# Performance work log

Hardware: AMD Instinct MI355X
Metric: run time of the kernel (lower is better)

## Reference

```python
import jax, jax.numpy as jnp
import numpy as np

DIM = 256

def setup_inputs() -> dict:
    key = jax.random.key(0)
    ks = jax.random.split(key, 7)
    B, S, D = 8, 4096, DIM
    scale = 1.0 / np.sqrt(D)
    x = jax.random.normal(ks[0], (B, S, D), dtype=jnp.float32)
    # torch Linear: y = x @ W.T + b, W is [out, in]
    Wq = jax.random.normal(ks[1], (D, D), dtype=jnp.float32) * scale
    Wk = jax.random.normal(ks[2], (D, D), dtype=jnp.float32) * scale
    Wv = jax.random.normal(ks[3], (D, D), dtype=jnp.float32) * scale
    bq = jax.random.normal(ks[4], (D,), dtype=jnp.float32) * 0.01
    bk = jax.random.normal(ks[5], (D,), dtype=jnp.float32) * 0.01
    bv = jax.random.normal(ks[6], (D,), dtype=jnp.float32) * 0.01
    return {"x": x, "Wq": Wq, "bq": bq, "Wk": Wk, "bk": bk, "Wv": Wv, "bv": bv}

def reference(x, Wq, bq, Wk, bk, Wv, bv):
    D = x.shape[-1]
    scale = D ** -0.5
    q = jnp.einsum('bsd,ed->bse', x, Wq) + bq  # [B,S,D]
    k = jnp.einsum('bsd,ed->bse', x, Wk) + bk
    v = jnp.einsum('bsd,ed->bse', x, Wv) + bv
    attn = jnp.einsum('bqd,bkd->bqk', q, k) * scale  # [B,S,S]
    attn = jax.nn.softmax(attn, axis=-1)
    return x + jnp.einsum('bqk,bkd->bqd', attn, v)
```

## Files before the change

kernel.cpp:

```cpp
#include <hip/hip_runtime.h>
#include <hip/hip_bf16.h>

typedef __attribute__((ext_vector_type(8))) short bf16x8;
typedef __attribute__((ext_vector_type(4))) short short4v;
typedef __attribute__((ext_vector_type(4))) float f32x4;
typedef __attribute__((ext_vector_type(16))) float f32x16;

#define MFMA16(a, b, c) __builtin_amdgcn_mfma_f32_16x16x32_bf16(a, b, c, 0, 0, 0)
#define MFMA32(a, b, c) __builtin_amdgcn_mfma_f32_32x32x16_bf16(a, b, c, 0, 0, 0)

__device__ __forceinline__ short f2bf(float f) {
    union { __hip_bfloat16 h; short s; } u;
    u.h = __float2bfloat16(f);
    return u.s;
}

__device__ __forceinline__ bf16x8 cvt8(const float* __restrict__ p) {
    f32x4 a = *reinterpret_cast<const f32x4*>(p);
    f32x4 b = *reinterpret_cast<const f32x4*>(p + 4);
    bf16x8 r;
    r[0] = f2bf(a[0]); r[1] = f2bf(a[1]); r[2] = f2bf(a[2]); r[3] = f2bf(a[3]);
    r[4] = f2bf(b[0]); r[5] = f2bf(b[1]); r[6] = f2bf(b[2]); r[7] = f2bf(b[3]);
    return r;
}

typedef __attribute__((address_space(1))) const unsigned int g_u32;
typedef __attribute__((address_space(3))) unsigned int l_u32;
__device__ __forceinline__ void gld16(const void* g, void* l) {
    __builtin_amdgcn_global_load_lds((g_u32*)(g), (l_u32*)(l), 16, 0, 0);
}

#define SBAR()    asm volatile("s_barrier" ::: "memory")
#define VMCNT(N)  asm volatile("s_waitcnt vmcnt(" #N ")" ::: "memory")

__global__ void wcvt_kernel(const float* __restrict__ Wq, const float* __restrict__ Wk,
                            const float* __restrict__ Wv, short* __restrict__ Wb)
{
    int t = blockIdx.x * 256 + threadIdx.x;
    int out_row = t & 255;
    int h  = (t >> 8) & 1;
    int kc = (t >> 9) & 15;
    int proj = t >> 13;
    const float* src = (proj == 0 ? Wq : (proj == 1 ? Wk : Wv))
                     + out_row * 256 + kc * 16 + h * 8;
    *reinterpret_cast<bf16x8*>(Wb + t * 8) = cvt8(src);
}

__global__ __launch_bounds__(256, 2) void qkv_kernel(
    const float* __restrict__ x, const short* __restrict__ Wb,
    const float* __restrict__ bq, const float* __restrict__ bk, const float* __restrict__ bv,
    short* __restrict__ qo, short* __restrict__ ko, short* __restrict__ vto)
{
    const int wave = threadIdx.x >> 6, lane = threadIdx.x & 63;
    const int l31 = lane & 31, h = lane >> 5;
    const int row0 = blockIdx.x * 128;
    const int wrow = row0 + wave * 32;

    bf16x8 af[16];
    const float* __restrict__ xr = x + (size_t)(wrow + l31) * 256 + h * 8;
#pragma unroll
    for (int kc = 0; kc < 16; ++kc) af[kc] = cvt8(xr + kc * 16);

    __shared__ short tile[128][264];

    for (int proj = 0; proj < 3; ++proj) {
        const short* __restrict__ W = Wb + proj * 65536;
        const float* __restrict__ bias = proj == 0 ? bq : (proj == 1 ? bk : bv);

        f32x16 acc[8];
#pragma unroll
        for (int df = 0; df < 8; ++df)
#pragma unroll
            for (int e = 0; e < 16; ++e) acc[df][e] = 0.f;

#pragma unroll
        for (int kc = 0; kc < 16; ++kc)
#pragma unroll
            for (int df = 0; df < 8; ++df) {
                bf16x8 bfr = *reinterpret_cast<const bf16x8*>(
                    W + ((kc * 2 + h) * 256 + df * 32 + l31) * 8);
                acc[df] = MFMA32(af[kc], bfr, acc[df]);
            }

        if (proj < 2) {
            short* __restrict__ dst = proj == 0 ? qo : ko;
#pragma unroll
            for (int df = 0; df < 8; ++df) {
                int col = df * 32 + l31;
                float bv_ = bias[col];
#pragma unroll
                for (int rg = 0; rg < 16; ++rg) {
                    int r = (rg & 3) + 8 * (rg >> 2) + 4 * h;
                    dst[(size_t)(wrow + r) * 256 + col] = f2bf(acc[df][rg] + bv_);
                }
            }
        } else {
#pragma unroll
            for (int df = 0; df < 8; ++df) {
                int col = df * 32 + l31;
                float bv_ = bias[col];
#pragma unroll
                for (int rg = 0; rg < 16; ++rg) {
                    int r = (rg & 3) + 8 * (rg >> 2) + 4 * h;
                    tile[wave * 32 + r][col] = f2bf(acc[df][rg] + bv_);
                }
            }
            __syncthreads();
            int d = threadIdx.x;
            int bb = row0 >> 12, s0 = row0 & 4095;
            short* __restrict__ dst = vto + ((size_t)bb * 256 + d) * 4096 + s0;
#pragma unroll
            for (int i = 0; i < 16; ++i) {
                bf16x8 v;
#pragma unroll
                for (int j = 0; j < 8; ++j) {
                    int p  = i * 8 + j;
                    int kp = p & 63;
                    int key = (kp & 3) * 16 + (kp >> 2);
                    v[j] = tile[(p & 64) + key][d];
                }
                *reinterpret_cast<bf16x8*>(dst + i * 8) = v;
            }
        }
    }
}

__global__ __launch_bounds__(256, 2) void attn_kernel(
    const short* __restrict__ q, const short* __restrict__ k,
    const short* __restrict__ vt, const float* __restrict__ x,
    float* __restrict__ out)
{
    const int id = blockIdx.x;
    const int b = id & 7, qt = id >> 3;
    const int tid = threadIdx.x;
    const int wave = tid >> 6, lane = tid & 63;
    const int l15 = lane & 15, l4 = lane >> 4;
    const int qrow0 = qt * 64 + wave * 16;

    const short* __restrict__ qb = q  + (size_t)b * 4096 * 256;
    const short* __restrict__ kb = k  + (size_t)b * 4096 * 256;
    const short* __restrict__ vb = vt + (size_t)b * 256 * 4096;

    __shared__ short smem[32768];
    __shared__ short plds[4][16][72];
    short (*pw)[72] = plds[wave];

    bf16x8 qf[8];
    const short* __restrict__ qr = qb + (size_t)(qrow0 + l15) * 256 + l4 * 8;
#pragma unroll
    for (int kc = 0; kc < 8; ++kc)
        qf[kc] = *reinterpret_cast<const bf16x8*>(qr + kc * 32);

    f32x4 o[16];
#pragma unroll
    for (int df = 0; df < 16; ++df) { f32x4 z = {0.f,0.f,0.f,0.f}; o[df] = z; }

    float ls[4] = {0.f, 0.f, 0.f, 0.f};
    const float cs = 0.0625f * 1.44269504f;

#define STAGE(T)                                                               \
  { _Pragma("unroll")                                                          \
    for (int i = 0; i < 16; ++i) {                                             \
        int c = i * 256 + tid;                                                 \
        int ss = c & 63;                                                       \
        const short* src;                                                      \
        if (c < 2048) {                                                        \
            int nf = c >> 9, kc = (c >> 6) & 7;                                \
            src = kb + (size_t)((T) * 64 + nf * 16 + (ss & 15)) * 256          \
                     + kc * 32 + (ss >> 4) * 8;                                \
        } else {                                                               \
            int df = (c >> 7) & 15, kc2 = (c >> 6) & 1;                        \
            src = vb + (size_t)(df * 16 + (ss & 15)) * 4096 + (T) * 64         \
                     + kc2 * 32 + (ss >> 4) * 8;                               \
        }                                                                      \
        gld16(src, &smem[c * 8]);                                              \
    } }

    STAGE(0);
    VMCNT(0);
    SBAR();
    __builtin_amdgcn_sched_barrier(0);

    const short* __restrict__ kb2 = smem;
    const short* __restrict__ vb2 = smem + 16384;

    for (int t = 0; t < 64; ++t) {
        f32x4 sacc[4];
#pragma unroll
        for (int nf = 0; nf < 4; ++nf) { f32x4 z = {0.f,0.f,0.f,0.f}; sacc[nf] = z; }
#pragma unroll
        for (int nf = 0; nf < 4; ++nf)
#pragma unroll
            for (int kc = 0; kc < 8; ++kc) {
                bf16x8 kf = *reinterpret_cast<const bf16x8*>(
                    kb2 + (nf * 512 + kc * 64 + lane) * 8);
                sacc[nf] = MFMA16(qf[kc], kf, sacc[nf]);
            }

#pragma unroll
        for (int r = 0; r < 4; ++r) {
            short4v pk;
#pragma unroll
            for (int nf = 0; nf < 4; ++nf) {
                float p = exp2f(sacc[nf][r] * cs);
                ls[r] += p;
                pk[nf] = f2bf(p);
            }
            *reinterpret_cast<short4v*>(&pw[l4 * 4 + r][l15 * 4]) = pk;
        }
        bf16x8 pf0 = *reinterpret_cast<const bf16x8*>(&pw[l15][l4 * 8]);
        bf16x8 pf1 = *reinterpret_cast<const bf16x8*>(&pw[l15][32 + l4 * 8]);

#pragma unroll
        for (int df = 0; df < 16; ++df) {
            bf16x8 v0 = *reinterpret_cast<const bf16x8*>(
                vb2 + (df * 128 + lane) * 8);
            bf16x8 v1 = *reinterpret_cast<const bf16x8*>(
                vb2 + (df * 128 + 64 + lane) * 8);
            o[df] = MFMA16(pf0, v0, o[df]);
            o[df] = MFMA16(pf1, v1, o[df]);
        }

        SBAR();
        if (t < 63) {
            STAGE(t + 1);
            VMCNT(0);
        }
        SBAR();
        __builtin_amdgcn_sched_barrier(0);
    }

    float inv[4];
#pragma unroll
    for (int r = 0; r < 4; ++r) {
        float v = ls[r];
#pragma unroll
        for (int d = 1; d < 16; d <<= 1) v += __shfl_xor(v, d);
        inv[r] = 1.0f / v;
    }
#pragma unroll
    for (int r = 0; r < 4; ++r) {
        size_t row = (size_t)b * 4096 + qrow0 + l4 * 4 + r;
#pragma unroll
        for (int df = 0; df < 16; ++df) {
            int col = df * 16 + l15;
            out[row * 256 + col] = o[df][r] * inv[r] + x[row * 256 + col];
        }
    }
#undef STAGE
}

extern "C" void kernel_launch(void* const* d_in, const int* in_sizes, int n_in,
                              void* d_out, int out_size, void* d_ws, size_t ws_size,
                              hipStream_t stream) {
    const float* x  = (const float*)d_in[0];
    const float* Wq = (const float*)d_in[1];
    const float* bq = (const float*)d_in[2];
    const float* Wk = (const float*)d_in[3];
    const float* bk = (const float*)d_in[4];
    const float* Wv = (const float*)d_in[5];
    const float* bv = (const float*)d_in[6];
    float* out = (float*)d_out;

    char* ws = (char*)d_ws;
    short* qb  = (short*)ws;
    short* kb  = (short*)(ws + (size_t)16 * 1024 * 1024);
    short* vtb = (short*)(ws + (size_t)32 * 1024 * 1024);
    short* Wb  = (short*)d_out;

    wcvt_kernel<<<96, 256, 0, stream>>>(Wq, Wk, Wv, Wb);

    qkv_kernel<<<256, 256, 0, stream>>>(x, Wb, bq, bk, bv, qb, kb, vtb);

    attn_kernel<<<512, 256, 0, stream>>>(qb, kb, vtb, x, out);
}
```

Baseline: 315.1 us.

## Double-buffer K/V tiles and enlarge attention blocks to eight waves

The attention kernel now uses 512-thread blocks covering 128 query rows, so each K/V tile staged into LDS is shared by twice as many waves. Two LDS buffers alternate so the global-to-LDS load of the next tile is issued before computing on the current one, overlapping memory latency with MFMA work instead of stalling. This raises LDS use to about 146KB per block, limiting occupancy to one block per CU, and halves the grid.

After: 291.4 us. -7.5%, faster.

```diff
diff --git a/kernel.cpp b/kernel.cpp
--- a/kernel.cpp
+++ b/kernel.cpp
@@ -125,7 +125,7 @@
     }
 }
 
-__global__ __launch_bounds__(256, 2) void attn_kernel(
+__global__ __launch_bounds__(512, 2) void attn_kernel(
     const short* __restrict__ q, const short* __restrict__ k,
     const short* __restrict__ vt, const float* __restrict__ x,
     float* __restrict__ out)
@@ -135,14 +135,15 @@
     const int tid = threadIdx.x;
     const int wave = tid >> 6, lane = tid & 63;
     const int l15 = lane & 15, l4 = lane >> 4;
-    const int qrow0 = qt * 64 + wave * 16;
+    const int qrow0 = qt * 128 + wave * 16;
 
     const short* __restrict__ qb = q  + (size_t)b * 4096 * 256;
     const short* __restrict__ kb = k  + (size_t)b * 4096 * 256;
     const short* __restrict__ vb = vt + (size_t)b * 256 * 4096;
 
-    __shared__ short smem[32768];
-    __shared__ short plds[4][16][72];
+    __shared__ short smemA[32768];
+    __shared__ short smemB[32768];
+    __shared__ short plds[8][16][72];
     short (*pw)[72] = plds[wave];
 
     bf16x8 qf[8];
@@ -158,10 +159,10 @@
     float ls[4] = {0.f, 0.f, 0.f, 0.f};
     const float cs = 0.0625f * 1.44269504f;
 
-#define STAGE(T)                                                               \
+#define STAGE(T, BUF)                                                          \
   { _Pragma("unroll")                                                          \
-    for (int i = 0; i < 16; ++i) {                                             \
-        int c = i * 256 + tid;                                                 \
+    for (int i = 0; i < 8; ++i) {                                              \
+        int c = i * 512 + tid;                                                 \
         int ss = c & 63;                                                       \
         const short* src;                                                      \
         if (c < 2048) {                                                        \
@@ -173,59 +174,63 @@
             src = vb + (size_t)(df * 16 + (ss & 15)) * 4096 + (T) * 64         \
                      + kc2 * 32 + (ss >> 4) * 8;                               \
         }                                                                      \
-        gld16(src, &smem[c * 8]);                                              \
+        gld16(src, &BUF[c * 8]);                                               \
     } }
 
-    STAGE(0);
+#define COMPUTE(BUF)                                                           \
+  {                                                                            \
+    f32x4 sacc[4];                                                             \
+    _Pragma("unroll")                                                          \
+    for (int nf = 0; nf < 4; ++nf) { f32x4 z = {0.f,0.f,0.f,0.f}; sacc[nf] = z; } \
+    _Pragma("unroll")                                                          \
+    for (int nf = 0; nf < 4; ++nf)                                             \
+        _Pragma("unroll")                                                      \
+        for (int kc = 0; kc < 8; ++kc) {                                       \
+            bf16x8 kf = *reinterpret_cast<const bf16x8*>(                      \
+                BUF + (nf * 512 + kc * 64 + lane) * 8);                        \
+            sacc[nf] = MFMA16(qf[kc], kf, sacc[nf]);                           \
+        }                                                                      \
+    _Pragma("unroll")                                                          \
+    for (int r = 0; r < 4; ++r) {                                              \
+        short4v pk;                                                            \
+        _Pragma("unroll")                                                      \
+        for (int nf = 0; nf < 4; ++nf) {                                       \
+            float p = exp2f(sacc[nf][r] * cs);                                 \
+            ls[r] += p;                                                        \
+            pk[nf] = f2bf(p);                                                  \
+        }                                                                      \
+        *reinterpret_cast<short4v*>(&pw[l4 * 4 + r][l15 * 4]) = pk;            \
+    }                                                                          \
+    bf16x8 pf0 = *reinterpret_cast<const bf16x8*>(&pw[l15][l4 * 8]);           \
+    bf16x8 pf1 = *reinterpret_cast<const bf16x8*>(&pw[l15][32 + l4 * 8]);      \
+    _Pragma("unroll")                                                          \
+    for (int df = 0; df < 16; ++df) {                                          \
+        bf16x8 v0 = *reinterpret_cast<const bf16x8*>(                          \
+            BUF + 16384 + (df * 128 + lane) * 8);                              \
+        bf16x8 v1 = *reinterpret_cast<const bf16x8*>(                          \
+            BUF + 16384 + (df * 128 + 64 + lane) * 8);                         \
+        o[df] = MFMA16(pf0, v0, o[df]);                                        \
+        o[df] = MFMA16(pf1, v1, o[df]);                                        \
+    }                                                                          \
+  }
+
+    STAGE(0, smemA);
     VMCNT(0);
     SBAR();
     __builtin_amdgcn_sched_barrier(0);
 
-    const short* __restrict__ kb2 = smem;
-    const short* __restrict__ vb2 = smem + 16384;
-
-    for (int t = 0; t < 64; ++t) {
-        f32x4 sacc[4];
-#pragma unroll
-        for (int nf = 0; nf < 4; ++nf) { f32x4 z = {0.f,0.f,0.f,0.f}; sacc[nf] = z; }
-#pragma unroll
-        for (int nf = 0; nf < 4; ++nf)
-#pragma unroll
-            for (int kc = 0; kc < 8; ++kc) {
-                bf16x8 kf = *reinterpret_cast<const bf16x8*>(
-                    kb2 + (nf * 512 + kc * 64 + lane) * 8);
-                sacc[nf] = MFMA16(qf[kc], kf, sacc[nf]);
-            }
-
-#pragma unroll
-        for (int r = 0; r < 4; ++r) {
-            short4v pk;
-#pragma unroll
-            for (int nf = 0; nf < 4; ++nf) {
-                float p = exp2f(sacc[nf][r] * cs);
-                ls[r] += p;
-                pk[nf] = f2bf(p);
-            }
-            *reinterpret_cast<short4v*>(&pw[l4 * 4 + r][l15 * 4]) = pk;
-        }
-        bf16x8 pf0 = *reinterpret_cast<const bf16x8*>(&pw[l15][l4 * 8]);
-        bf16x8 pf1 = *reinterpret_cast<const bf16x8*>(&pw[l15][32 + l4 * 8]);
-
-#pragma unroll
-        for (int df = 0; df < 16; ++df) {
-            bf16x8 v0 = *reinterpret_cast<const bf16x8*>(
-                vb2 + (df * 128 + lane) * 8);
-            bf16x8 v1 = *reinterpret_cast<const bf16x8*>(
-                vb2 + (df * 128 + 64 + lane) * 8);
-            o[df] = MFMA16(pf0, v0, o[df]);
-            o[df] = MFMA16(pf1, v1, o[df]);
-        }
-
+    for (int tt = 0; tt < 32; ++tt) {
+        const int t0 = 2 * tt, t1 = 2 * tt + 1;
+
+        STAGE(t0 + 1, smemB);
+        COMPUTE(smemA);
+        VMCNT(0);
         SBAR();
-        if (t < 63) {
-            STAGE(t + 1);
-            VMCNT(0);
-        }
+        __builtin_amdgcn_sched_barrier(0);
+
+        if (t1 < 63) STAGE(t1 + 1, smemA);
+        COMPUTE(smemB);
+        if (t1 < 63) VMCNT(0);
         SBAR();
         __builtin_amdgcn_sched_barrier(0);
     }
@@ -248,6 +253,7 @@
         }
     }
 #undef STAGE
+#undef COMPUTE
 }
 
 extern "C" void kernel_launch(void* const* d_in, const int* in_sizes, int n_in,
@@ -272,5 +278,5 @@
 
     qkv_kernel<<<256, 256, 0, stream>>>(x, Wb, bq, bk, bv, qb, kb, vtb);
 
-    attn_kernel<<<512, 256, 0, stream>>>(qb, kb, vtb, x, out);
-}
+    attn_kernel<<<256, 512, 0, stream>>>(qb, kb, vtb, x, out);
+}
```
